# Performance work log

Hardware: AMD Instinct MI355X
Metric: run time of the kernel (lower is better)

## Reference

```python
import jax, jax.numpy as jnp
import numpy as np

H = 8  # num_heads

def setup_inputs() -> dict:
    key = jax.random.key(0)
    ks = jax.random.split(key, 8)
    N, B, E = 1024, 8, 256
    value = jax.random.normal(ks[0], (N, B, E), dtype=jnp.float32)
    pos = jax.random.normal(ks[1], (B * H, N, N), dtype=jnp.float32)
    s = 1.0 / np.sqrt(E)
    in_proj_w = jax.random.uniform(ks[2], (3 * E, E), jnp.float32, -s, s)   # content attn qkv proj
    in_proj_b = jnp.zeros((3 * E,), jnp.float32)
    out_w = jax.random.uniform(ks[3], (E, E), jnp.float32, -s, s)
    out_b = jnp.zeros((E,), jnp.float32)
    return {"value": value, "position_attention_weights": pos,
            "in_proj_w": in_proj_w, "in_proj_b": in_proj_b,
            "out_w": out_w, "out_b": out_b}

def reference(value, position_attention_weights, in_proj_w, in_proj_b, out_w, out_b):
    # value: (N, B, E) seq-first, position_attention_weights: (B*H, N, N)
    N, B, E = value.shape
    Dh = E // H
    qkv = value @ in_proj_w.T + in_proj_b            # (N, B, 3E)
    q, k, v = jnp.split(qkv, 3, axis=-1)
    # (N, B, E) -> (B*H, N, Dh)
    def to_heads(t):
        return t.reshape(N, B * H, Dh).transpose(1, 0, 2)
    q, k, v = to_heads(q), to_heads(k), to_heads(v)
    scale = 1.0 / jnp.sqrt(jnp.asarray(Dh, q.dtype))
    content = jnp.einsum('bnd,bmd->bnm', q * scale, k)   # (B*H, N, N) content scores
    # merge_attention == 'gate': clamp both, log-sigmoid gate on positional, add
    content = jnp.clip(content, -10.0, 10.0)
    pos = jnp.clip(position_attention_weights, -10.0, 10.0)
    scores = jax.nn.log_sigmoid(pos) + content
    attn = jax.nn.softmax(scores, axis=-1)               # normalizer
    out = jnp.einsum('bnm,bmd->bnd', attn, v)            # (B*H, N, Dh)
    out = out.transpose(1, 0, 2).reshape(N, B, E)        # back to (N, B, E)
    out = out @ out_w.T + out_b
    attn_avg = attn.reshape(B, H, N, N).mean(axis=1)     # averaged attention weights
    return out, attn_avg
```

## Files before the change

kernel.cpp:

```cpp
#include <hip/hip_runtime.h>
#include <hip/hip_bf16.h>

typedef __attribute__((ext_vector_type(8))) short short8;
typedef __attribute__((ext_vector_type(4))) float f32x4;
typedef __attribute__((ext_vector_type(4))) unsigned short u16x4;

#define MFMA16(a,b,c) __builtin_amdgcn_mfma_f32_16x16x32_bf16((a),(b),(c),0,0,0)

__device__ __forceinline__ ushort f2bf(float x) {
  union { float f; unsigned u; } v; v.f = x;
  unsigned u = v.u;
  u = (u + 0x7fffu + ((u >> 16) & 1u)) >> 16;
  return (ushort)u;
}

__device__ __forceinline__ short8 ld8(const ushort* p) {
  return *reinterpret_cast<const short8*>(p);
}

__global__ void conv_kernel(const float* __restrict__ value,
                            const float* __restrict__ w_in,
                            const float* __restrict__ w_out,
                            ushort* __restrict__ vbf,
                            ushort* __restrict__ wbf,
                            ushort* __restrict__ owbf) {
  int i = blockIdx.x * 256 + threadIdx.x;
  const float* src; ushort* dst; int j;
  if (i < 524288)      { src = value; dst = vbf;  j = i; }
  else if (i < 573440) { src = w_in;  dst = wbf;  j = i - 524288; }
  else                 { src = w_out; dst = owbf; j = i - 573440; }
  float4 v = reinterpret_cast<const float4*>(src)[j];
  u16x4 o;
  o[0] = f2bf(v.x); o[1] = f2bf(v.y); o[2] = f2bf(v.z); o[3] = f2bf(v.w);
  reinterpret_cast<u16x4*>(dst)[j] = o;
}

__global__ __launch_bounds__(256) void qkv_kernel(
    const ushort* __restrict__ vbf, const ushort* __restrict__ wbf,
    const float* __restrict__ bias,
    ushort* __restrict__ qh, ushort* __restrict__ kh, ushort* __restrict__ vt) {
  int tid = threadIdx.x;
  int wave = tid >> 6, lane = tid & 63;
  int lq = lane & 15, lg = lane >> 4;
  int r0 = blockIdx.x * 16;
  int c0 = (blockIdx.y * 4 + wave) * 16;
  f32x4 acc = {0.f, 0.f, 0.f, 0.f};
  const ushort* ap = vbf + (size_t)(r0 + lq) * 256 + lg * 8;
  const ushort* bp = wbf + (size_t)(c0 + lq) * 256 + lg * 8;
#pragma unroll
  for (int k0 = 0; k0 < 256; k0 += 32)
    acc = MFMA16(ld8(ap + k0), ld8(bp + k0), acc);
  int c = c0 + lq;
  float bv = bias[c];
#pragma unroll
  for (int r = 0; r < 4; ++r) {
    int row = r0 + lg * 4 + r;
    int n = row >> 3, b = row & 7;
    float v = acc[r] + bv;
    if (c < 256) {
      int h = c >> 5, d = c & 31;
      qh[((size_t)(b * 8 + h) * 1024 + n) * 32 + d] = f2bf(v * 0.17677669529663689f);
    } else if (c < 512) {
      int cc = c - 256, h = cc >> 5, d = cc & 31;
      kh[((size_t)(b * 8 + h) * 1024 + n) * 32 + d] = f2bf(v);
    } else {
      int cc = c - 512, h = cc >> 5, d = cc & 31;
      vt[((size_t)(b * 8 + h) * 32 + d) * 1024 + n] = f2bf(v);
    }
  }
}

__global__ __launch_bounds__(512, 4) void attn_kernel(
    const ushort* __restrict__ qh, const ushort* __restrict__ kh,
    const ushort* __restrict__ vt, const float* __restrict__ pos,
    ushort* __restrict__ ao, float* __restrict__ avg_out) {
  __shared__ __align__(16) unsigned char smem[16 * 1028 * 2 + 16 * 8 * 4];
  ushort (*attn_lds)[1028] = reinterpret_cast<ushort(*)[1028]>(smem);
  float  (*pvred)[16][32]  = reinterpret_cast<float(*)[16][32]>(smem);
  float  (*rowsumT)[8]     = reinterpret_cast<float(*)[8]>(smem + 16 * 1028 * 2);

  int tid = threadIdx.x;
  int wave = tid >> 6, lane = tid & 63;
  int lq = lane & 15, lg = lane >> 4;
  int n0 = blockIdx.x * 16;
  int b = blockIdx.y;
  int mb = wave * 128;

  float avg[8][4];
#pragma unroll
  for (int t = 0; t < 8; ++t)
#pragma unroll
    for (int r = 0; r < 4; ++r) avg[t][r] = 0.f;

  for (int h = 0; h < 8; ++h) {
    int bh = b * 8 + h;
    short8 qa = ld8(qh + ((size_t)bh * 1024 + n0 + lq) * 32 + lg * 8);
    const ushort* kp = kh + (size_t)bh * 32768 + lg * 8;
    f32x4 S[8];
#pragma unroll
    for (int t = 0; t < 8; ++t) {
      f32x4 z = {0.f, 0.f, 0.f, 0.f};
      S[t] = MFMA16(qa, ld8(kp + (size_t)(mb + lq * 8 + t) * 32), z);
    }
    const float* pp = pos + (size_t)bh * 1048576;
    float rs[4] = {0.f, 0.f, 0.f, 0.f};
#pragma unroll
    for (int r = 0; r < 4; ++r) {
      int n = n0 + lg * 4 + r;
      const float* rowp = pp + (size_t)n * 1024 + mb + lq * 8;
      float4 p0 = *reinterpret_cast<const float4*>(rowp);
      float4 p1 = *reinterpret_cast<const float4*>(rowp + 4);
      float pv[8] = {p0.x, p0.y, p0.z, p0.w, p1.x, p1.y, p1.z, p1.w};
#pragma unroll
      for (int t = 0; t < 8; ++t) {
        float p = fminf(10.f, fmaxf(-10.f, pv[t]));
        float c = fminf(10.f, fmaxf(-10.f, S[t][r]));
        float w = __expf(c - 10.f) * __builtin_amdgcn_rcpf(1.f + __expf(-p));
        S[t][r] = w;
        rs[r] += w;
      }
    }
#pragma unroll
    for (int r = 0; r < 4; ++r) {
      rs[r] += __shfl_xor(rs[r], 1);
      rs[r] += __shfl_xor(rs[r], 2);
      rs[r] += __shfl_xor(rs[r], 4);
      rs[r] += __shfl_xor(rs[r], 8);
    }
    if (lq == 0) {
#pragma unroll
      for (int r = 0; r < 4; ++r) rowsumT[lg * 4 + r][wave] = rs[r];
    }
    __syncthreads();
    float inv[4];
#pragma unroll
    for (int r = 0; r < 4; ++r) {
      int row = lg * 4 + r;
      float4 a0 = *reinterpret_cast<const float4*>(&rowsumT[row][0]);
      float4 a1 = *reinterpret_cast<const float4*>(&rowsumT[row][4]);
      inv[r] = __builtin_amdgcn_rcpf(a0.x + a0.y + a0.z + a0.w +
                                     a1.x + a1.y + a1.z + a1.w);
    }
#pragma unroll
    for (int r = 0; r < 4; ++r) {
      int row = lg * 4 + r;
      short8 pk;
#pragma unroll
      for (int t = 0; t < 8; ++t) {
        float a = S[t][r] * inv[r];
        avg[t][r] += a;
        pk[t] = (short)f2bf(a);
      }
      *reinterpret_cast<short8*>(&attn_lds[row][mb + lq * 8]) = pk;
    }
    __syncthreads();
    f32x4 acc0 = {0.f, 0.f, 0.f, 0.f}, acc1 = {0.f, 0.f, 0.f, 0.f};
    const ushort* vp = vt + (size_t)bh * 32768 + mb + lg * 8;
#pragma unroll
    for (int ks = 0; ks < 4; ++ks) {
      short8 pa = *reinterpret_cast<const short8*>(&attn_lds[lq][mb + ks * 32 + lg * 8]);
      acc0 = MFMA16(pa, ld8(vp + (size_t)lq * 1024 + ks * 32), acc0);
      acc1 = MFMA16(pa, ld8(vp + (size_t)(lq + 16) * 1024 + ks * 32), acc1);
    }
    __syncthreads();
#pragma unroll
    for (int r = 0; r < 4; ++r) {
      pvred[wave][lg * 4 + r][lq] = acc0[r];
      pvred[wave][lg * 4 + r][lq + 16] = acc1[r];
    }
    __syncthreads();
    {
      int n = tid >> 5, d = tid & 31;
      float s = 0.f;
#pragma unroll
      for (int w = 0; w < 8; ++w) s += pvred[w][n][d];
      ao[((size_t)(n0 + n) * 8 + b) * 256 + h * 32 + d] = f2bf(s);
    }
  }
#pragma unroll
  for (int r = 0; r < 4; ++r) {
    int n = n0 + lg * 4 + r;
    float* op = avg_out + (size_t)b * 1048576 + (size_t)n * 1024 + mb + lq * 8;
    float4 v0 = {avg[0][r] * 0.125f, avg[1][r] * 0.125f, avg[2][r] * 0.125f, avg[3][r] * 0.125f};
    float4 v1 = {avg[4][r] * 0.125f, avg[5][r] * 0.125f, avg[6][r] * 0.125f, avg[7][r] * 0.125f};
    *reinterpret_cast<float4*>(op) = v0;
    *reinterpret_cast<float4*>(op + 4) = v1;
  }
}

__global__ __launch_bounds__(256) void oproj_kernel(
    const ushort* __restrict__ ao, const ushort* __restrict__ owbf,
    const float* __restrict__ ob, float* __restrict__ outp) {
  int tid = threadIdx.x;
  int wave = tid >> 6, lane = tid & 63;
  int lq = lane & 15, lg = lane >> 4;
  int r0 = blockIdx.x * 16;
  int c0 = (blockIdx.y * 4 + wave) * 16;
  f32x4 acc = {0.f, 0.f, 0.f, 0.f};
  const ushort* ap = ao + (size_t)(r0 + lq) * 256 + lg * 8;
  const ushort* bp = owbf + (size_t)(c0 + lq) * 256 + lg * 8;
#pragma unroll
  for (int k0 = 0; k0 < 256; k0 += 32)
    acc = MFMA16(ld8(ap + k0), ld8(bp + k0), acc);
  int c = c0 + lq;
  float bv = ob[c];
#pragma unroll
  for (int r = 0; r < 4; ++r) {
    int row = r0 + lg * 4 + r;
    outp[(size_t)row * 256 + c] = acc[r] + bv;
  }
}

extern "C" void kernel_launch(void* const* d_in, const int* in_sizes, int n_in,
                              void* d_out, int out_size, void* d_ws, size_t ws_size,
                              hipStream_t stream) {
  const float* value = (const float*)d_in[0];
  const float* pos   = (const float*)d_in[1];
  const float* w_in  = (const float*)d_in[2];
  const float* b_in  = (const float*)d_in[3];
  const float* w_out = (const float*)d_in[4];
  const float* b_out = (const float*)d_in[5];

  char* ws = (char*)d_ws;
  ushort* vbf  = (ushort*)(ws);
  ushort* wbf  = (ushort*)(ws + 4194304);
  ushort* owbf = (ushort*)(ws + 4587520);
  ushort* qh   = (ushort*)(ws + 4718592);
  ushort* kh   = (ushort*)(ws + 8912896);
  ushort* vt   = (ushort*)(ws + 13107200);
  ushort* ao   = (ushort*)(ws + 17301504);

  float* outp = (float*)d_out;
  float* avgp = outp + 2097152;

  conv_kernel<<<2304, 256, 0, stream>>>(value, w_in, w_out, vbf, wbf, owbf);
  qkv_kernel<<<dim3(512, 12), 256, 0, stream>>>(vbf, wbf, b_in, qh, kh, vt);
  attn_kernel<<<dim3(64, 8), 512, 0, stream>>>(qh, kh, vt, pos, ao, avgp);
  oproj_kernel<<<dim3(512, 4), 256, 0, stream>>>(ao, owbf, b_out, outp);
}
```

Baseline: 181.8 us.

## Defer softmax normalization past PV, swizzle LDS, add separate V transpose kernel

Unnormalized exp weights are packed to bf16 and written to LDS before the row-sum reduction, and the PV MFMAs run right away, with the 1/rowsum applied to the PV accumulators afterward. This removes two barriers per head and lets the reduction overlap the matmul. The score computation is split into two halves to lower register pressure, and LDS columns are XOR-swizzled to reduce bank conflicts. V is now written row-major by the QKV kernel and transposed by a new small kernel rather than scattered with strided stores. One side effect is that the averaged attention output is now built from bf16-rounded weights, which lowers its precision.

Result: no change. 181.8 us (-0.0%).

```diff
diff --git a/kernel.cpp b/kernel.cpp
--- a/kernel.cpp
+++ b/kernel.cpp
@@ -12,6 +12,11 @@
   unsigned u = v.u;
   u = (u + 0x7fffu + ((u >> 16) & 1u)) >> 16;
   return (ushort)u;
+}
+
+__device__ __forceinline__ float bf2f(ushort u) {
+  union { unsigned u; float f; } v; v.u = ((unsigned)u) << 16;
+  return v.f;
 }
 
 __device__ __forceinline__ short8 ld8(const ushort* p) {
@@ -38,7 +43,7 @@
 __global__ __launch_bounds__(256) void qkv_kernel(
     const ushort* __restrict__ vbf, const ushort* __restrict__ wbf,
     const float* __restrict__ bias,
-    ushort* __restrict__ qh, ushort* __restrict__ kh, ushort* __restrict__ vt) {
+    ushort* __restrict__ qh, ushort* __restrict__ kh, ushort* __restrict__ vv) {
   int tid = threadIdx.x;
   int wave = tid >> 6, lane = tid & 63;
   int lq = lane & 15, lg = lane >> 4;
@@ -65,19 +70,35 @@
       kh[((size_t)(b * 8 + h) * 1024 + n) * 32 + d] = f2bf(v);
     } else {
       int cc = c - 512, h = cc >> 5, d = cc & 31;
-      vt[((size_t)(b * 8 + h) * 32 + d) * 1024 + n] = f2bf(v);
-    }
-  }
+      vv[((size_t)(b * 8 + h) * 1024 + n) * 32 + d] = f2bf(v);
+    }
+  }
+}
+
+__global__ __launch_bounds__(256) void vtrans_kernel(const ushort* __restrict__ vv,
+                                                     ushort* __restrict__ vt) {
+  __shared__ ushort t[32][73];
+  int tid = threadIdx.x;
+  int bh = blockIdx.y, m0 = blockIdx.x * 64;
+  int mm = tid >> 2, d0 = (tid & 3) * 8;
+  short8 v = ld8(vv + ((size_t)bh * 1024 + m0 + mm) * 32 + d0);
+#pragma unroll
+  for (int j = 0; j < 8; ++j) t[d0 + j][mm] = (ushort)v[j];
+  __syncthreads();
+  int d = tid >> 3, mg = (tid & 7) * 8;
+  short8 o;
+#pragma unroll
+  for (int j = 0; j < 8; ++j) o[j] = (short)t[d][mg + j];
+  *reinterpret_cast<short8*>(vt + ((size_t)bh * 32 + d) * 1024 + m0 + mg) = o;
 }
 
 __global__ __launch_bounds__(512, 4) void attn_kernel(
     const ushort* __restrict__ qh, const ushort* __restrict__ kh,
     const ushort* __restrict__ vt, const float* __restrict__ pos,
     ushort* __restrict__ ao, float* __restrict__ avg_out) {
-  __shared__ __align__(16) unsigned char smem[16 * 1028 * 2 + 16 * 8 * 4];
-  ushort (*attn_lds)[1028] = reinterpret_cast<ushort(*)[1028]>(smem);
-  float  (*pvred)[16][32]  = reinterpret_cast<float(*)[16][32]>(smem);
-  float  (*rowsumT)[8]     = reinterpret_cast<float(*)[8]>(smem + 16 * 1028 * 2);
+  __shared__ __align__(16) ushort attn_lds[16][1028];
+  __shared__ float pvred[8][16][32];
+  __shared__ float rowsumT[16][8];
 
   int tid = threadIdx.x;
   int wave = tid >> 6, lane = tid & 63;
@@ -96,29 +117,59 @@
     int bh = b * 8 + h;
     short8 qa = ld8(qh + ((size_t)bh * 1024 + n0 + lq) * 32 + lg * 8);
     const ushort* kp = kh + (size_t)bh * 32768 + lg * 8;
-    f32x4 S[8];
-#pragma unroll
-    for (int t = 0; t < 8; ++t) {
-      f32x4 z = {0.f, 0.f, 0.f, 0.f};
-      S[t] = MFMA16(qa, ld8(kp + (size_t)(mb + lq * 8 + t) * 32), z);
-    }
-    const float* pp = pos + (size_t)bh * 1048576;
+    const float* pp = pos + ((size_t)bh << 20);
     float rs[4] = {0.f, 0.f, 0.f, 0.f};
-#pragma unroll
-    for (int r = 0; r < 4; ++r) {
-      int n = n0 + lg * 4 + r;
-      const float* rowp = pp + (size_t)n * 1024 + mb + lq * 8;
-      float4 p0 = *reinterpret_cast<const float4*>(rowp);
-      float4 p1 = *reinterpret_cast<const float4*>(rowp + 4);
-      float pv[8] = {p0.x, p0.y, p0.z, p0.w, p1.x, p1.y, p1.z, p1.w};
-#pragma unroll
-      for (int t = 0; t < 8; ++t) {
-        float p = fminf(10.f, fmaxf(-10.f, pv[t]));
-        float c = fminf(10.f, fmaxf(-10.f, S[t][r]));
-        float w = __expf(c - 10.f) * __builtin_amdgcn_rcpf(1.f + __expf(-p));
-        S[t][r] = w;
-        rs[r] += w;
-      }
+    short8 wreg[4];
+
+    {
+      f32x4 S[4];
+#pragma unroll
+      for (int t = 0; t < 4; ++t) {
+        f32x4 z = {0.f, 0.f, 0.f, 0.f};
+        S[t] = MFMA16(qa, ld8(kp + (size_t)(mb + lq * 8 + t) * 32), z);
+      }
+#pragma unroll
+      for (int r = 0; r < 4; ++r) {
+        int n = n0 + lg * 4 + r;
+        float4 p0 = *reinterpret_cast<const float4*>(pp + (size_t)n * 1024 + mb + lq * 8);
+        float pv[4] = {p0.x, p0.y, p0.z, p0.w};
+#pragma unroll
+        for (int t = 0; t < 4; ++t) {
+          float p = fminf(10.f, fmaxf(-10.f, pv[t]));
+          float c = fminf(10.f, fmaxf(-10.f, S[t][r]));
+          float w = __expf(c - 10.f) * __builtin_amdgcn_rcpf(1.f + __expf(-p));
+          rs[r] += w;
+          wreg[r][t] = (short)f2bf(w);
+        }
+      }
+    }
+    {
+      f32x4 S[4];
+#pragma unroll
+      for (int t = 0; t < 4; ++t) {
+        f32x4 z = {0.f, 0.f, 0.f, 0.f};
+        S[t] = MFMA16(qa, ld8(kp + (size_t)(mb + lq * 8 + 4 + t) * 32), z);
+      }
+#pragma unroll
+      for (int r = 0; r < 4; ++r) {
+        int n = n0 + lg * 4 + r;
+        float4 p1 = *reinterpret_cast<const float4*>(pp + (size_t)n * 1024 + mb + lq * 8 + 4);
+        float pv[4] = {p1.x, p1.y, p1.z, p1.w};
+#pragma unroll
+        for (int t = 0; t < 4; ++t) {
+          float p = fminf(10.f, fmaxf(-10.f, pv[t]));
+          float c = fminf(10.f, fmaxf(-10.f, S[t][r]));
+          float w = __expf(c - 10.f) * __builtin_amdgcn_rcpf(1.f + __expf(-p));
+          rs[r] += w;
+          wreg[r][4 + t] = (short)f2bf(w);
+        }
+      }
+    }
+#pragma unroll
+    for (int r = 0; r < 4; ++r) {
+      int row = lg * 4 + r;
+      int col = (mb + lq * 8) ^ ((row & 7) << 3);
+      *reinterpret_cast<short8*>(&attn_lds[row][col]) = wreg[r];
     }
 #pragma unroll
     for (int r = 0; r < 4; ++r) {
@@ -130,6 +181,15 @@
     if (lq == 0) {
 #pragma unroll
       for (int r = 0; r < 4; ++r) rowsumT[lg * 4 + r][wave] = rs[r];
+    }
+    f32x4 acc0 = {0.f, 0.f, 0.f, 0.f}, acc1 = {0.f, 0.f, 0.f, 0.f};
+    const ushort* vp = vt + (size_t)bh * 32768 + mb + lg * 8;
+#pragma unroll
+    for (int ks = 0; ks < 4; ++ks) {
+      int col = (mb + ks * 32 + lg * 8) ^ ((lq & 7) << 3);
+      short8 pa = *reinterpret_cast<const short8*>(&attn_lds[lq][col]);
+      acc0 = MFMA16(pa, ld8(vp + (size_t)lq * 1024 + ks * 32), acc0);
+      acc1 = MFMA16(pa, ld8(vp + (size_t)(lq + 16) * 1024 + ks * 32), acc1);
     }
     __syncthreads();
     float inv[4];
@@ -144,30 +204,14 @@
 #pragma unroll
     for (int r = 0; r < 4; ++r) {
       int row = lg * 4 + r;
-      short8 pk;
-#pragma unroll
-      for (int t = 0; t < 8; ++t) {
-        float a = S[t][r] * inv[r];
-        avg[t][r] += a;
-        pk[t] = (short)f2bf(a);
-      }
-      *reinterpret_cast<short8*>(&attn_lds[row][mb + lq * 8]) = pk;
-    }
-    __syncthreads();
-    f32x4 acc0 = {0.f, 0.f, 0.f, 0.f}, acc1 = {0.f, 0.f, 0.f, 0.f};
-    const ushort* vp = vt + (size_t)bh * 32768 + mb + lg * 8;
-#pragma unroll
-    for (int ks = 0; ks < 4; ++ks) {
-      short8 pa = *reinterpret_cast<const short8*>(&attn_lds[lq][mb + ks * 32 + lg * 8]);
-      acc0 = MFMA16(pa, ld8(vp + (size_t)lq * 1024 + ks * 32), acc0);
-      acc1 = MFMA16(pa, ld8(vp + (size_t)(lq + 16) * 1024 + ks * 32), acc1);
-    }
-    __syncthreads();
-#pragma unroll
-    for (int r = 0; r < 4; ++r) {
-      pvred[wave][lg * 4 + r][lq] = acc0[r];
-      pvred[wave][lg * 4 + r][lq + 16] = acc1[r];
-    }
+      pvred[wave][row][lq] = acc0[r] * inv[r];
+      pvred[wave][row][lq + 16] = acc1[r] * inv[r];
+    }
+#pragma unroll
+    for (int r = 0; r < 4; ++r)
+#pragma unroll
+      for (int t = 0; t < 8; ++t)
+        avg[t][r] += bf2f((ushort)wreg[r][t]) * inv[r];
     __syncthreads();
     {
       int n = tid >> 5, d = tid & 31;
@@ -227,14 +271,16 @@
   ushort* owbf = (ushort*)(ws + 4587520);
   ushort* qh   = (ushort*)(ws + 4718592);
   ushort* kh   = (ushort*)(ws + 8912896);
-  ushort* vt   = (ushort*)(ws + 13107200);
+  ushort* vv   = (ushort*)(ws + 13107200);
+  ushort* vt   = (ushort*)(ws);
   ushort* ao   = (ushort*)(ws + 17301504);
 
   float* outp = (float*)d_out;
   float* avgp = outp + 2097152;
 
   conv_kernel<<<2304, 256, 0, stream>>>(value, w_in, w_out, vbf, wbf, owbf);
-  qkv_kernel<<<dim3(512, 12), 256, 0, stream>>>(vbf, wbf, b_in, qh, kh, vt);
+  qkv_kernel<<<dim3(512, 12), 256, 0, stream>>>(vbf, wbf, b_in, qh, kh, vv);
+  vtrans_kernel<<<dim3(16, 64), 256, 0, stream>>>(vv, vt);
   attn_kernel<<<dim3(64, 8), 512, 0, stream>>>(qh, kh, vt, pos, ao, avgp);
   oproj_kernel<<<dim3(512, 4), 256, 0, stream>>>(ao, owbf, b_out, outp);
 }
```
